# Kernel optimization log

Hardware: AMD Instinct MI355X
Metric: run time of the kernel (lower is better)

## Reference

```python
import jax, jax.numpy as jnp
import numpy as np

G = 4096        # graphs
NPG = 32        # nodes per graph
N = G * NPG     # total nodes
D = 256         # hidden (inv node feat) dim
SH = 256        # shared / node-MLP hidden dim
HDG = 50        # graph head dim
HDN = 3         # node head dim
NB = 2          # num branches (dataset IDs)


def setup_inputs() -> dict:
    key = jax.random.key(0)
    ks = jax.random.split(key, 8)
    s = 0.02
    return {
        "x": jax.random.normal(ks[0], (N, D), jnp.float32),
        "dataset_name": jax.random.randint(ks[1], (G,), 0, NB, jnp.int32),
        "batch": (jnp.arange(N) // NPG).astype(jnp.int32),
        "Wgs": jax.random.normal(ks[2], (NB, D, SH), jnp.float32) * s,
        "bgs": jnp.zeros((NB, SH), jnp.float32),
        "Wgh": jax.random.normal(ks[3], (NB, SH, 2 * HDG), jnp.float32) * s,
        "bgh": jnp.zeros((NB, 2 * HDG), jnp.float32),
        "Wn1": jax.random.normal(ks[4], (NB, D, SH), jnp.float32) * s,
        "bn1": jnp.zeros((NB, SH), jnp.float32),
        "Wn2": jax.random.normal(ks[5], (NB, SH, 2 * HDN), jnp.float32) * s,
        "bn2": jnp.zeros((NB, 2 * HDN), jnp.float32),
    }


def reference(x, dataset_name, batch, Wgs, bgs, Wgh, bgh, Wn1, bn1, Wn2, bn2):
    n_nodes = x.shape[0]
    n_graphs = dataset_name.shape[0]

    # ---- graph pooling (mean) : scatter-reduce nodes -> graphs ----
    counts = jax.ops.segment_sum(jnp.ones((n_nodes,), x.dtype), batch, num_segments=n_graphs)
    x_graph = jax.ops.segment_sum(x, batch, num_segments=n_graphs) / counts[:, None]  # [G, D]

    # ---- graph head: per-branch shared MLP + head, then branch dispatch ----
    hg = jax.nn.relu(jnp.einsum("gd,bds->bgs", x_graph, Wgs) + bgs[:, None, :])       # [B, G, SH]
    og = jnp.einsum("bgs,bsh->bgh", hg, Wgh) + bgh[:, None, :]                        # [B, G, 2*HDG]
    out_g = og[dataset_name, jnp.arange(n_graphs)]                                    # [G, 2*HDG]
    g_head = out_g[:, :HDG]
    g_var = out_g[:, HDG:] ** 2

    # ---- node head (mlp type): per-branch MLP on nodes, dispatch by node's graph ID ----
    node_branch = dataset_name[batch]                                                 # [N]
    hn = jax.nn.relu(jnp.einsum("nd,bds->bns", x, Wn1) + bn1[:, None, :])             # [B, N, SH]
    on = jnp.einsum("bns,bsh->bnh", hn, Wn2) + bn2[:, None, :]                        # [B, N, 2*HDN]
    out_n = on[node_branch, jnp.arange(n_nodes)]                                      # [N, 2*HDN]
    n_head = out_n[:, :HDN]
    n_var = out_n[:, HDN:] ** 2

    # (outputs, outputs_var) flattened: heads then variance heads
    return (g_head, n_head, g_var, n_var)
```

## Files before the change

kernel.cpp:

```cpp
#include <hip/hip_runtime.h>
#include <hip/hip_bf16.h>


#define G_   4096
#define NPG_ 32
#define NN_  (G_*NPG_)
#define D_   256
#define SH_  256
#define HDG_ 50
#define HDN_ 3

#define OFF_GH 0
#define OFF_NH (G_*HDG_)
#define OFF_GV (OFF_NH + NN_*HDN_)
#define OFF_NV (OFF_GV + G_*HDG_)

typedef short v8s __attribute__((ext_vector_type(8)));
typedef short v4s __attribute__((ext_vector_type(4)));
typedef float v4f __attribute__((ext_vector_type(4)));

__device__ __forceinline__ float bfu2f(unsigned short u) {
    return __uint_as_float(((unsigned int)u) << 16);
}
__device__ __forceinline__ unsigned short f2bfu(float v) {
    __hip_bfloat16 b = __float2bfloat16(v);
    return *reinterpret_cast<unsigned short*>(&b);
}

#define MFMA16(a, b, c) __builtin_amdgcn_mfma_f32_16x16x32_bf16((a), (b), (c), 0, 0, 0)

__global__ __launch_bounds__(256) void wpack(const float* __restrict__ Wn1,
                                             const float* __restrict__ Wgs,
                                             const float* __restrict__ Wgh,
                                             const float* __restrict__ Wn2,
                                             unsigned short* __restrict__ out) {
    const int idx = blockIdx.x * 256 + threadIdx.x;
    float v;
    if (idx < 131072) {
        const int b = idx >> 16, rem = idx & 65535, s = rem >> 8, d = rem & 255;
        v = Wn1[b * 65536 + d * 256 + s];
    } else if (idx < 262144) {
        const int i2 = idx - 131072;
        const int np = i2 >> 8, d = i2 & 255;
        v = Wgs[(np >> 8) * 65536 + d * 256 + (np & 255)];
    } else if (idx < 327680) {
        const int i3 = idx - 262144;
        const int npp = i3 >> 8, k = i3 & 255;
        const int b = npp >> 7, c = npp & 127;
        v = (c < 100) ? Wgh[b * 25600 + k * 100 + c] : 0.f;
    } else {
        const int i4 = idx - 327680;
        const int b = i4 >> 12, rem = i4 & 4095, n = rem >> 8, k = rem & 255;
        v = (n < 6) ? Wn2[b * 1536 + k * 6 + n] : 0.f;
    }
    out[idx] = f2bfu(v);
}

__global__ void build_glist(const int* __restrict__ dsname,
                            int* __restrict__ glist,
                            int* __restrict__ gcnt) {
    __shared__ int cnt[2];
    const int t = threadIdx.x;
    if (t < 2) cnt[t] = 0;
    __syncthreads();
    for (int i = 0; i < 16; i++) {
        const int g = i * 256 + t;
        const int b = dsname[g];
        const int slot = atomicAdd(&cnt[b], 1);
        glist[b * G_ + slot] = g;
    }
    __syncthreads();
    if (t < 2) gcnt[t] = cnt[t];
}

__global__ __launch_bounds__(512) void node_pers(const float* __restrict__ x,
                                                 const int* __restrict__ glist,
                                                 const int* __restrict__ gcnt,
                                                 const unsigned short* __restrict__ Wn1T,
                                                 const float* __restrict__ bn1,
                                                 const unsigned short* __restrict__ Wn2b,
                                                 const float* __restrict__ bn2,
                                                 unsigned short* __restrict__ xg,
                                                 float* __restrict__ out) {
    __shared__ __align__(16) unsigned short xs[NPG_ * 264];
    __shared__ __align__(16) float red[8 * 256];
    const int t = threadIdx.x;
    const int wave = t >> 6, lane = t & 63;
    const int l15 = lane & 15, quad = lane >> 4;
    const int br = blockIdx.x & 1;
    const int bslot = blockIdx.x >> 1;
    const int cnt = gcnt[br];

    const int base_n = (wave & 1) * 128 + (wave >> 1) * 32;

    v8s B1[2][8];
    float bias1[2];
    #pragma unroll
    for (int nt = 0; nt < 2; nt++) {
        const unsigned short* bp = Wn1T + br * 65536 + (base_n + nt * 16 + l15) * 256 + quad * 8;
        #pragma unroll
        for (int kt = 0; kt < 8; kt++) B1[nt][kt] = *(const v8s*)(bp + kt * 32);
        bias1[nt] = bn1[br * 256 + base_n + nt * 16 + l15];
    }

    v8s B2[4];
    if (wave < 4) {
        const int kh = wave >> 1;
        const unsigned short* bp = Wn2b + br * 4096 + l15 * 256 + kh * 128 + quad * 8;
        #pragma unroll
        for (int j = 0; j < 4; j++) B2[j] = *(const v8s*)(bp + j * 32);
    }
    float bias2 = 0.f; int i2 = 0, c2 = 0;
    if (t < 192) { i2 = t / 6; c2 = t % 6; bias2 = bn2[br * 6 + c2]; }

    const int rb = t >> 6;
    const int colb = (t & 63) * 4;

    int gi = bslot;
    int g = glist[br * G_ + ((gi < cnt) ? gi : (cnt - 1))];
    float4 pv[4];
    #pragma unroll
    for (int k = 0; k < 4; k++)
        pv[k] = *(const float4*)(x + (size_t)g * 8192 + (rb * 4 + k) * 256 + colb);

    for (; gi < cnt; gi += 128) {
        const int gcur = g;
        float s0 = 0.f, s1 = 0.f, s2 = 0.f, s3 = 0.f;
        #pragma unroll
        for (int k = 0; k < 4; k++) {
            s0 += pv[k].x; s1 += pv[k].y; s2 += pv[k].z; s3 += pv[k].w;
            v4s bv; bv[0] = (short)f2bfu(pv[k].x); bv[1] = (short)f2bfu(pv[k].y);
                    bv[2] = (short)f2bfu(pv[k].z); bv[3] = (short)f2bfu(pv[k].w);
            *(v4s*)(&xs[(rb * 4 + k) * 264 + colb]) = bv;
        }
        *(float4*)(&red[rb * 256 + colb]) = make_float4(s0, s1, s2, s3);

        {
            const int gi2 = gi + 128;
            const int gn = glist[br * G_ + ((gi2 < cnt) ? gi2 : (cnt - 1))];
            #pragma unroll
            for (int k = 0; k < 4; k++)
                pv[k] = *(const float4*)(x + (size_t)gn * 8192 + (rb * 4 + k) * 256 + colb);
            g = gn;
        }
        __syncthreads();

        if (t < 256) {
            float m = 0.f;
            #pragma unroll
            for (int r = 0; r < 8; r++) m += red[r * 256 + t];
            xg[(size_t)gcur * 256 + t] = f2bfu(m * (1.0f / NPG_));
        }

        v4f acc[2][2];
        #pragma unroll
        for (int mt = 0; mt < 2; mt++)
            #pragma unroll
            for (int nt = 0; nt < 2; nt++) acc[mt][nt] = (v4f){0.f, 0.f, 0.f, 0.f};
        #pragma unroll
        for (int kt = 0; kt < 8; kt++) {
            const int ko = kt * 32;
            v8s a0 = *(const v8s*)(&xs[l15 * 264 + quad * 8 + ko]);
            v8s a1 = *(const v8s*)(&xs[(16 + l15) * 264 + quad * 8 + ko]);
            #pragma unroll
            for (int nt = 0; nt < 2; nt++) {
                acc[0][nt] = MFMA16(a0, B1[nt][kt], acc[0][nt]);
                acc[1][nt] = MFMA16(a1, B1[nt][kt], acc[1][nt]);
            }
        }
        __syncthreads();

        #pragma unroll
        for (int nt = 0; nt < 2; nt++) {
            const int col = base_n + nt * 16 + l15;
            #pragma unroll
            for (int mt = 0; mt < 2; mt++)
                #pragma unroll
                for (int r = 0; r < 4; r++) {
                    const int row = mt * 16 + quad * 4 + r;
                    const float v = acc[mt][nt][r] + bias1[nt];
                    xs[row * 264 + col] = f2bfu(v > 0.f ? v : 0.f);
                }
        }
        __syncthreads();

        if (wave < 4) {
            const int mtl = wave & 1, kh = wave >> 1;
            v4f a2 = (v4f){0.f, 0.f, 0.f, 0.f};
            #pragma unroll
            for (int j = 0; j < 4; j++) {
                const int ko = kh * 128 + j * 32;
                v8s av = *(const v8s*)(&xs[(mtl * 16 + l15) * 264 + ko + quad * 8]);
                a2 = MFMA16(av, B2[j], a2);
            }
            #pragma unroll
            for (int r = 0; r < 4; r++)
                red[kh * 512 + (mtl * 16 + quad * 4 + r) * 16 + l15] = a2[r];
        }
        __syncthreads();

        if (t < 192) {
            const float o = red[i2 * 16 + c2] + red[512 + i2 * 16 + c2] + bias2;
            const int n = gcur * NPG_ + i2;
            if (c2 < HDN_) out[OFF_NH + n * HDN_ + c2] = o;
            else           out[OFF_NV + n * HDN_ + (c2 - HDN_)] = o * o;
        }
        __syncthreads();
    }
}

__global__ __launch_bounds__(256) void graph_mfma2(const unsigned short* __restrict__ xg,
                                                   const int* __restrict__ dsname,
                                                   const unsigned short* __restrict__ WgsT,
                                                   const float* __restrict__ bgs,
                                                   const unsigned short* __restrict__ WghP,
                                                   const float* __restrict__ bgh,
                                                   float* __restrict__ out) {
    __shared__ __align__(16) unsigned short xs[32 * 264];
    __shared__ int bls[32];
    const int gbase = blockIdx.x * 32;
    const int t = threadIdx.x;
    const int wave = t >> 6, lane = t & 63;
    const int l15 = lane & 15, quad = lane >> 4;
    if (t < 32) bls[t] = dsname[gbase + t];

    #pragma unroll
    for (int k = 0; k < 4; k++) {
        const int flat = k * 2048 + t * 8;
        *(v8s*)(&xs[(flat >> 8) * 264 + (flat & 255)]) =
            *(const v8s*)(xg + (size_t)gbase * 256 + flat);
    }
    __syncthreads();

    v4f acc[2][8];
    #pragma unroll
    for (int mt = 0; mt < 2; mt++)
        #pragma unroll
        for (int nt = 0; nt < 8; nt++) acc[mt][nt] = (v4f){0.f, 0.f, 0.f, 0.f};

    const unsigned short* Ab = &xs[l15 * 264 + quad * 8];
    const unsigned short* Bb = WgsT + (wave * 128 + l15) * 256 + quad * 8;

    #pragma unroll
    for (int kt = 0; kt < 8; kt++) {
        const int ko = kt * 32;
        v8s a0 = *(const v8s*)(Ab + ko);
        v8s a1 = *(const v8s*)(Ab + 16 * 264 + ko);
        #pragma unroll
        for (int nt = 0; nt < 8; nt++) {
            v8s bv = *(const v8s*)(Bb + nt * 16 * 256 + ko);
            acc[0][nt] = MFMA16(a0, bv, acc[0][nt]);
            acc[1][nt] = MFMA16(a1, bv, acc[1][nt]);
        }
    }
    __syncthreads();

    {
        const int bw = wave >> 1;
        #pragma unroll
        for (int nt = 0; nt < 8; nt++) {
            const int sp = wave * 128 + nt * 16 + l15;
            const int s_local = sp & 255;
            const float bias = bgs[sp];
            #pragma unroll
            for (int mt = 0; mt < 2; mt++)
                #pragma unroll
                for (int r = 0; r < 4; r++) {
                    const int row = mt * 16 + quad * 4 + r;
                    if (bls[row] == bw) {
                        const float v = acc[mt][nt][r] + bias;
                        xs[row * 264 + s_local] = f2bfu(v > 0.f ? v : 0.f);
                    }
                }
        }
    }
    __syncthreads();

    v4f acc2[2][4];
    #pragma unroll
    for (int mt = 0; mt < 2; mt++)
        #pragma unroll
        for (int nt = 0; nt < 4; nt++) acc2[mt][nt] = (v4f){0.f, 0.f, 0.f, 0.f};

    const unsigned short* B2 = WghP + ((wave * 4) * 16 + l15) * 256 + quad * 8;
    #pragma unroll
    for (int kt = 0; kt < 8; kt++) {
        const int ko = kt * 32;
        v8s a0 = *(const v8s*)(&xs[l15 * 264 + ko + quad * 8]);
        v8s a1 = *(const v8s*)(&xs[(16 + l15) * 264 + ko + quad * 8]);
        #pragma unroll
        for (int nt = 0; nt < 4; nt++) {
            v8s bv = *(const v8s*)(B2 + nt * 16 * 256 + ko);
            acc2[0][nt] = MFMA16(a0, bv, acc2[0][nt]);
            acc2[1][nt] = MFMA16(a1, bv, acc2[1][nt]);
        }
    }

    #pragma unroll
    for (int nt = 0; nt < 4; nt++) {
        const int npp  = (wave * 4 + nt) * 16 + l15;
        const int bo   = npp >> 7, c = npp & 127;
        if (c < 2 * HDG_) {
            const float bias = bgh[bo * 2 * HDG_ + c];
            #pragma unroll
            for (int mt = 0; mt < 2; mt++)
                #pragma unroll
                for (int r = 0; r < 4; r++) {
                    const int row = mt * 16 + quad * 4 + r;
                    if (bls[row] == bo) {
                        const float o = acc2[mt][nt][r] + bias;
                        const int g = gbase + row;
                        if (c < HDG_) out[OFF_GH + g * HDG_ + c] = o;
                        else          out[OFF_GV + g * HDG_ + (c - HDG_)] = o * o;
                    }
                }
        }
    }
}

extern "C" void kernel_launch(void* const* d_in, const int* in_sizes, int n_in,
                              void* d_out, int out_size, void* d_ws, size_t ws_size,
                              hipStream_t stream) {
    const float* x      = (const float*)d_in[0];
    const int*   dsname = (const int*)d_in[1];
    const float* Wgs = (const float*)d_in[3];
    const float* bgs = (const float*)d_in[4];
    const float* Wgh = (const float*)d_in[5];
    const float* bgh = (const float*)d_in[6];
    const float* Wn1 = (const float*)d_in[7];
    const float* bn1 = (const float*)d_in[8];
    const float* Wn2 = (const float*)d_in[9];
    const float* bn2 = (const float*)d_in[10];
    float* out = (float*)d_out;

    unsigned short* wsbuf = (unsigned short*)d_ws;
    unsigned short* Wn1T  = wsbuf;
    unsigned short* WgsT  = wsbuf + 131072;
    unsigned short* WghP  = wsbuf + 262144;
    unsigned short* Wn2b  = wsbuf + 327680;
    unsigned short* xg    = wsbuf + 335872;
    int* glist = (int*)((char*)d_ws + 2768896);
    int* gcnt  = (int*)((char*)d_ws + 2801664);

    wpack      <<<1312,    256, 0, stream>>>(Wn1, Wgs, Wgh, Wn2, wsbuf);
    build_glist<<<1,       256, 0, stream>>>(dsname, glist, gcnt);
    node_pers  <<<256,     512, 0, stream>>>(x, glist, gcnt, Wn1T, bn1, Wn2b, bn2, xg, out);
    graph_mfma2<<<G_ / 32, 256, 0, stream>>>(xg, dsname, WgsT, bgs, WghP, bgh, out);
}
```

Baseline: 245.1 us.

## Double node-kernel grid, split second GEMM across all waves, parallelize graph list

Doubles the node kernel's grid to 512 persistent blocks, so each branch is served by twice as many blocks and each block loops over fewer graphs. It adds a separate LDS buffer for the hidden activations, which lets two of the per-iteration barriers be removed. The second small GEMM is spread over all eight waves with a four-way partial reduction, instead of only four waves doing the work. The single-block graph-list builder becomes 16 blocks using global atomics, with the counters zeroed inside the weight-packing kernel. The costs are more LDS per block, which may limit occupancy, and a nondeterministic order of graphs in the list.

```diff
diff --git a/kernel.cpp b/kernel.cpp
--- a/kernel.cpp
+++ b/kernel.cpp
@@ -33,7 +33,9 @@
                                              const float* __restrict__ Wgs,
                                              const float* __restrict__ Wgh,
                                              const float* __restrict__ Wn2,
-                                             unsigned short* __restrict__ out) {
+                                             unsigned short* __restrict__ out,
+                                             int* __restrict__ gcnt) {
+    if (blockIdx.x == 0 && threadIdx.x < 2) gcnt[threadIdx.x] = 0;
     const int idx = blockIdx.x * 256 + threadIdx.x;
     float v;
     if (idx < 131072) {
@@ -56,34 +58,28 @@
     out[idx] = f2bfu(v);
 }
 
-__global__ void build_glist(const int* __restrict__ dsname,
-                            int* __restrict__ glist,
-                            int* __restrict__ gcnt) {
-    __shared__ int cnt[2];
-    const int t = threadIdx.x;
-    if (t < 2) cnt[t] = 0;
-    __syncthreads();
-    for (int i = 0; i < 16; i++) {
-        const int g = i * 256 + t;
-        const int b = dsname[g];
-        const int slot = atomicAdd(&cnt[b], 1);
-        glist[b * G_ + slot] = g;
-    }
-    __syncthreads();
-    if (t < 2) gcnt[t] = cnt[t];
-}
-
-__global__ __launch_bounds__(512) void node_pers(const float* __restrict__ x,
-                                                 const int* __restrict__ glist,
-                                                 const int* __restrict__ gcnt,
-                                                 const unsigned short* __restrict__ Wn1T,
-                                                 const float* __restrict__ bn1,
-                                                 const unsigned short* __restrict__ Wn2b,
-                                                 const float* __restrict__ bn2,
-                                                 unsigned short* __restrict__ xg,
-                                                 float* __restrict__ out) {
+__global__ __launch_bounds__(256) void build_glist16(const int* __restrict__ dsname,
+                                                     int* __restrict__ glist,
+                                                     int* __restrict__ gcnt) {
+    const int g = blockIdx.x * 256 + threadIdx.x;
+    const int b = dsname[g];
+    const int slot = atomicAdd(&gcnt[b], 1);
+    glist[b * G_ + slot] = g;
+}
+
+__global__ __launch_bounds__(512, 4) void node_pers2(const float* __restrict__ x,
+                                                     const int* __restrict__ glist,
+                                                     const int* __restrict__ gcnt,
+                                                     const unsigned short* __restrict__ Wn1T,
+                                                     const float* __restrict__ bn1,
+                                                     const unsigned short* __restrict__ Wn2b,
+                                                     const float* __restrict__ bn2,
+                                                     unsigned short* __restrict__ xg,
+                                                     float* __restrict__ out) {
     __shared__ __align__(16) unsigned short xs[NPG_ * 264];
+    __shared__ __align__(16) unsigned short hb[NPG_ * 264];
     __shared__ __align__(16) float red[8 * 256];
+    __shared__ __align__(16) float red2[4 * 512];
     const int t = threadIdx.x;
     const int wave = t >> 6, lane = t & 63;
     const int l15 = lane & 15, quad = lane >> 4;
@@ -103,12 +99,12 @@
         bias1[nt] = bn1[br * 256 + base_n + nt * 16 + l15];
     }
 
-    v8s B2[4];
-    if (wave < 4) {
-        const int kh = wave >> 1;
-        const unsigned short* bp = Wn2b + br * 4096 + l15 * 256 + kh * 128 + quad * 8;
-        #pragma unroll
-        for (int j = 0; j < 4; j++) B2[j] = *(const v8s*)(bp + j * 32);
+    const int kh = wave >> 1, mtl = wave & 1;
+    v8s B2[2];
+    {
+        const unsigned short* bp = Wn2b + br * 4096 + l15 * 256 + kh * 64 + quad * 8;
+        B2[0] = *(const v8s*)(bp);
+        B2[1] = *(const v8s*)(bp + 32);
     }
     float bias2 = 0.f; int i2 = 0, c2 = 0;
     if (t < 192) { i2 = t / 6; c2 = t % 6; bias2 = bn2[br * 6 + c2]; }
@@ -117,13 +113,13 @@
     const int colb = (t & 63) * 4;
 
     int gi = bslot;
-    int g = glist[br * G_ + ((gi < cnt) ? gi : (cnt - 1))];
+    int g = glist[br * G_ + ((gi < cnt) ? gi : (cnt > 0 ? cnt - 1 : 0))];
     float4 pv[4];
     #pragma unroll
     for (int k = 0; k < 4; k++)
         pv[k] = *(const float4*)(x + (size_t)g * 8192 + (rb * 4 + k) * 256 + colb);
 
-    for (; gi < cnt; gi += 128) {
+    for (; gi < cnt; gi += 256) {
         const int gcur = g;
         float s0 = 0.f, s1 = 0.f, s2 = 0.f, s3 = 0.f;
         #pragma unroll
@@ -136,7 +132,7 @@
         *(float4*)(&red[rb * 256 + colb]) = make_float4(s0, s1, s2, s3);
 
         {
-            const int gi2 = gi + 128;
+            const int gi2 = gi + 256;
             const int gn = glist[br * G_ + ((gi2 < cnt) ? gi2 : (cnt - 1))];
             #pragma unroll
             for (int k = 0; k < 4; k++)
@@ -168,7 +164,6 @@
                 acc[1][nt] = MFMA16(a1, B1[nt][kt], acc[1][nt]);
             }
         }
-        __syncthreads();
 
         #pragma unroll
         for (int nt = 0; nt < 2; nt++) {
@@ -179,33 +174,31 @@
                 for (int r = 0; r < 4; r++) {
                     const int row = mt * 16 + quad * 4 + r;
                     const float v = acc[mt][nt][r] + bias1[nt];
-                    xs[row * 264 + col] = f2bfu(v > 0.f ? v : 0.f);
+                    hb[row * 264 + col] = f2bfu(v > 0.f ? v : 0.f);
                 }
         }
         __syncthreads();
 
-        if (wave < 4) {
-            const int mtl = wave & 1, kh = wave >> 1;
+        {
             v4f a2 = (v4f){0.f, 0.f, 0.f, 0.f};
-            #pragma unroll
-            for (int j = 0; j < 4; j++) {
-                const int ko = kh * 128 + j * 32;
-                v8s av = *(const v8s*)(&xs[(mtl * 16 + l15) * 264 + ko + quad * 8]);
-                a2 = MFMA16(av, B2[j], a2);
-            }
+            const int kb = kh * 64 + quad * 8;
+            v8s av0 = *(const v8s*)(&hb[(mtl * 16 + l15) * 264 + kb]);
+            v8s av1 = *(const v8s*)(&hb[(mtl * 16 + l15) * 264 + kb + 32]);
+            a2 = MFMA16(av0, B2[0], a2);
+            a2 = MFMA16(av1, B2[1], a2);
             #pragma unroll
             for (int r = 0; r < 4; r++)
-                red[kh * 512 + (mtl * 16 + quad * 4 + r) * 16 + l15] = a2[r];
+                red2[kh * 512 + (mtl * 16 + quad * 4 + r) * 16 + l15] = a2[r];
         }
         __syncthreads();
 
         if (t < 192) {
-            const float o = red[i2 * 16 + c2] + red[512 + i2 * 16 + c2] + bias2;
+            const float o = red2[i2 * 16 + c2] + red2[512 + i2 * 16 + c2]
+                          + red2[1024 + i2 * 16 + c2] + red2[1536 + i2 * 16 + c2] + bias2;
             const int n = gcur * NPG_ + i2;
             if (c2 < HDN_) out[OFF_NH + n * HDN_ + c2] = o;
             else           out[OFF_NV + n * HDN_ + (c2 - HDN_)] = o * o;
         }
-        __syncthreads();
     }
 }
 
@@ -342,8 +335,8 @@
     int* glist = (int*)((char*)d_ws + 2768896);
     int* gcnt  = (int*)((char*)d_ws + 2801664);
 
-    wpack      <<<1312,    256, 0, stream>>>(Wn1, Wgs, Wgh, Wn2, wsbuf);
-    build_glist<<<1,       256, 0, stream>>>(dsname, glist, gcnt);
-    node_pers  <<<256,     512, 0, stream>>>(x, glist, gcnt, Wn1T, bn1, Wn2b, bn2, xg, out);
-    graph_mfma2<<<G_ / 32, 256, 0, stream>>>(xg, dsname, WgsT, bgs, WghP, bgh, out);
-}
+    wpack        <<<1312,    256, 0, stream>>>(Wn1, Wgs, Wgh, Wn2, wsbuf, gcnt);
+    build_glist16<<<16,      256, 0, stream>>>(dsname, glist, gcnt);
+    node_pers2   <<<512,     512, 0, stream>>>(x, glist, gcnt, Wn1T, bn1, Wn2b, bn2, xg, out);
+    graph_mfma2  <<<G_ / 32, 256, 0, stream>>>(xg, dsname, WgsT, bgs, WghP, bgh, out);
+}
```

New measurement: 281.4 us. +14.8%, slower.
